# Kernel optimization log

Measured on AMD Instinct MI355X. Metric: run time of the kernel, lower is better.

## Reference

```python
import jax, jax.numpy as jnp
import numpy as np

N_ORDER = 13  # grid_size(10) + spline_order(3)
D_MODEL = 1024
HIDDEN = 2048
Z_DIM = 32
SEQ_LEN = 4096
IN0 = 2 * D_MODEL + Z_DIM  # 2080
RMS_EPS = 1e-6


def _kan_layer(x, base_w, poly_w, rms_scale):
    """KAN layer with Chebyshev basis, bf16 matmuls, fp32 RMSNorm.
    x: (..., in); base_w: (in,out); poly_w: (n_order,in,out); rms_scale: (out,)
    """
    prefix = x.shape[:-1]
    x2 = x.reshape(-1, x.shape[-1])
    out = jax.nn.silu(x2.astype(jnp.bfloat16)) @ base_w.astype(jnp.bfloat16)
    x_safe = jnp.tanh(x2.astype(jnp.float32))
    pw = poly_w.astype(jnp.bfloat16)
    T_prev = jnp.ones_like(x_safe)
    T_curr = x_safe
    out = out + T_prev.astype(jnp.bfloat16) @ pw[0]
    out = out + T_curr.astype(jnp.bfloat16) @ pw[1]
    for k in range(2, N_ORDER):
        T_next = 2.0 * x_safe * T_curr - T_prev
        out = out + T_next.astype(jnp.bfloat16) @ pw[k]
        T_prev, T_curr = T_curr, T_next
    o = out.astype(jnp.float32)
    o = o * jax.lax.rsqrt(jnp.mean(o * o, axis=-1, keepdims=True) + RMS_EPS) * rms_scale
    return o.reshape(prefix + (o.shape[-1],))


def setup_inputs() -> dict:
    key = jax.random.key(0)
    ks = jax.random.split(key, 10)
    B, N_tgt, S_ctx = 8, 2048, 128
    h_x = jax.random.normal(ks[0], (B, S_ctx, D_MODEL), dtype=jnp.float32)
    target_positions = jax.random.randint(ks[1], (B, N_tgt), 0, SEQ_LEN)
    z = jax.random.normal(ks[2], (B, N_tgt, Z_DIM), dtype=jnp.float32)
    pos_embed_w = jax.random.normal(ks[3], (SEQ_LEN, D_MODEL), dtype=jnp.float32) * 0.02
    base0 = jax.random.normal(ks[4], (IN0, HIDDEN), dtype=jnp.float32) * (1.0 / np.sqrt(IN0))
    poly0 = jax.random.normal(ks[5], (N_ORDER, IN0, HIDDEN), dtype=jnp.float32) * (0.1 / np.sqrt(IN0 * N_ORDER))
    rms0 = jnp.ones((HIDDEN,), dtype=jnp.float32)
    base1 = jax.random.normal(ks[6], (HIDDEN, D_MODEL), dtype=jnp.float32) * (1.0 / np.sqrt(HIDDEN))
    poly1 = jax.random.normal(ks[7], (N_ORDER, HIDDEN, D_MODEL), dtype=jnp.float32) * (0.1 / np.sqrt(HIDDEN * N_ORDER))
    rms1 = jnp.ones((D_MODEL,), dtype=jnp.float32)
    return {"h_x": h_x, "target_positions": target_positions, "z": z,
            "pos_embed_w": pos_embed_w, "base0": base0, "poly0": poly0, "rms0": rms0,
            "base1": base1, "poly1": poly1, "rms1": rms1}


def reference(h_x, target_positions, z, pos_embed_w, base0, poly0, rms0, base1, poly1, rms1):
    B = h_x.shape[0]
    N_tgt = target_positions.shape[1]
    ctx = jnp.broadcast_to(h_x[:, -1:, :], (B, N_tgt, D_MODEL))
    pos = pos_embed_w[target_positions]          # (B, N_tgt, d_model)
    x = jnp.concatenate([ctx, pos, z], axis=-1)  # (B, N_tgt, 2*d_model + z_dim)
    x = _kan_layer(x, base0, poly0, rms0)
    x = _kan_layer(x, base1, poly1, rms1)
    return x
```

## Files before the change

kernel.cpp:

```cpp
#include <hip/hip_runtime.h>
#include <hip/hip_bf16.h>
#include <math.h>

#define B_SZ 8
#define NT 2048
#define M_TOT (B_SZ * NT)
#define DM 1024
#define ZD 32
#define IN0 2080
#define HID 2048
#define OUT1 1024
#define NCH 13
#define PZ 1056
#define KPZ (NCH * PZ)
#define KCTX (NCH * DM)
#define K1 (NCH * HID)
#define RMS_EPS 1e-6f

typedef __bf16 bf16;
typedef __bf16 bf16x4 __attribute__((ext_vector_type(4)));
typedef __bf16 bf16x8 __attribute__((ext_vector_type(8)));
typedef float f32x4 __attribute__((ext_vector_type(4)));

__device__ __forceinline__ void gload16(const void* g, void* l) {
    __builtin_amdgcn_global_load_lds(
        (const __attribute__((address_space(1))) void*)g,
        (__attribute__((address_space(3))) void*)l, 16, 0, 0);
}

__device__ __forceinline__ float rb(float x) { return (float)(bf16)x; }

__device__ __forceinline__ unsigned pk2(float lo, float hi) {
    return (__builtin_bit_cast(unsigned, hi) & 0xFFFF0000u) |
           (__builtin_bit_cast(unsigned, lo) >> 16);
}
__device__ __forceinline__ float up_lo(unsigned u) { return __builtin_bit_cast(float, u << 16); }
__device__ __forceinline__ float up_hi(unsigned u) { return __builtin_bit_cast(float, u & 0xFFFF0000u); }

__global__ __launch_bounds__(256) void convert_w0(const float* __restrict__ base,
                                                  const float* __restrict__ poly,
                                                  bf16* __restrict__ wctx,
                                                  bf16* __restrict__ wposz) {
    __shared__ float tile[32][33];
    int c = blockIdx.z;
    const float* src = (c == 0) ? base : (poly + (size_t)c * IN0 * HID);
    int i0 = blockIdx.x * 32, n0 = blockIdx.y * 32;
    int tx = threadIdx.x, ty = threadIdx.y;
#pragma unroll
    for (int r = 0; r < 4; r++)
        tile[ty + r * 8][tx] = src[(size_t)(i0 + ty + r * 8) * HID + n0 + tx];
    __syncthreads();
#pragma unroll
    for (int r = 0; r < 4; r++) {
        int n = n0 + ty + r * 8;
        int i = i0 + tx;
        bf16 v = (bf16)tile[tx][ty + r * 8];
        if (i < 1024) wctx[(size_t)n * KCTX + (size_t)c * 1024 + i] = v;
        else          wposz[(size_t)n * KPZ + (size_t)c * PZ + (i - 1024)] = v;
    }
}

__global__ __launch_bounds__(256) void convert_w(const float* __restrict__ base,
                                                 const float* __restrict__ poly,
                                                 bf16* __restrict__ dst, int IN, int OUT) {
    __shared__ float tile[32][33];
    int c = blockIdx.z;
    const float* src = (c == 0) ? base : (poly + (size_t)c * IN * OUT);
    int i0 = blockIdx.x * 32, n0 = blockIdx.y * 32;
    int tx = threadIdx.x, ty = threadIdx.y;
#pragma unroll
    for (int r = 0; r < 4; r++)
        tile[ty + r * 8][tx] = src[(size_t)(i0 + ty + r * 8) * OUT + n0 + tx];
    __syncthreads();
    size_t ldd = (size_t)NCH * IN;
#pragma unroll
    for (int r = 0; r < 4; r++) {
        int n = n0 + ty + r * 8;
        int i = i0 + tx;
        dst[(size_t)n * ldd + (size_t)c * IN + i] = (bf16)tile[tx][ty + r * 8];
    }
}

__global__ void col_sum_s1(const float* __restrict__ w, float* __restrict__ partial,
                           int IN, int OUT) {
    __shared__ float sm[4][64];
    int tx = threadIdx.x, ty = threadIdx.y;
    int n = blockIdx.x * 64 + tx;
    int s = blockIdx.y;
    float acc = 0.f;
    for (int i = 4 * s + ty; i < IN; i += 128) acc += (float)(bf16)w[(size_t)i * OUT + n];
    sm[ty][tx] = acc;
    __syncthreads();
    if (ty == 0) partial[(size_t)s * OUT + n] = sm[0][tx] + sm[1][tx] + sm[2][tx] + sm[3][tx];
}
__global__ void col_sum_s2(const float* __restrict__ partial, float* __restrict__ bias, int OUT) {
    int n = blockIdx.x * 256 + threadIdx.x;
    if (n >= OUT) return;
    float s = 0.f;
#pragma unroll
    for (int k = 0; k < 32; k++) s += partial[(size_t)k * OUT + n];
    bias[n] = s;
}

__device__ __forceinline__ void write_features4(bf16* __restrict__ row, int i,
                                                float4 o, int stride) {
    float x[4] = {o.x, o.y, o.z, o.w};
    bf16x4 t;
#pragma unroll
    for (int l = 0; l < 4; l++) {
        float xb = rb(x[l]);
        float e  = rb(expf(-xb));
        float d  = rb(1.f + e);
        float sg = rb(1.f / d);
        t[l] = (bf16)(xb * sg);
    }
    *(bf16x4*)&row[i] = t;
    float xs[4], Tp[4], Tc[4];
#pragma unroll
    for (int l = 0; l < 4; l++) {
        xs[l] = tanhf(x[l]);
        Tp[l] = 1.f; Tc[l] = xs[l];
        t[l] = (bf16)xs[l];
    }
    *(bf16x4*)&row[(size_t)stride + i] = t;
#pragma unroll
    for (int k = 2; k < NCH; k++) {
#pragma unroll
        for (int l = 0; l < 4; l++) {
            float Tn = 2.f * xs[l] * Tc[l] - Tp[l];
            t[l] = (bf16)Tn;
            Tp[l] = Tc[l]; Tc[l] = Tn;
        }
        *(bf16x4*)&row[(size_t)k * stride + i] = t;
    }
}

__global__ __launch_bounds__(256) void build_fctx(const float* __restrict__ h_x,
                                                  bf16* __restrict__ Fctx) {
    int id = blockIdx.x * 256 + threadIdx.x;
    int b = id >> 8;
    int i = (id & 255) * 4;
    float4 v = *(const float4*)&h_x[((size_t)b * 128 + 127) * DM + i];
    write_features4(Fctx + (size_t)b * KCTX, i, v, DM);
}

__global__ void ctx_dot(const bf16* __restrict__ Fctx, const bf16* __restrict__ wctx,
                        float* __restrict__ ctx_part) {
    __shared__ float sm[4][64];
    int tx = threadIdx.x, ty = threadIdx.y;
    int n = blockIdx.x * 64 + tx;
    int c = blockIdx.y, b = blockIdx.z;
    const bf16* f = Fctx + ((size_t)b * NCH + c) * DM;
    const bf16* wv = wctx + (size_t)n * KCTX + (size_t)c * DM;
    float s = 0.f;
    for (int i = ty; i < DM; i += 4) s += (float)f[i] * (float)wv[i];
    sm[ty][tx] = s;
    __syncthreads();
    if (ty == 0) ctx_part[((size_t)b * NCH + c) * HID + n] = sm[0][tx] + sm[1][tx] + sm[2][tx] + sm[3][tx];
}

__global__ __launch_bounds__(256) void build_fposz(const int* __restrict__ tp,
                                                   const float* __restrict__ z,
                                                   const float* __restrict__ pe,
                                                   bf16* __restrict__ F) {
    int id = blockIdx.x * 256 + threadIdx.x;
    if (id >= M_TOT * (PZ / 4)) return;
    int ml = id / (PZ / 4);
    int i = (id - ml * (PZ / 4)) * 4;
    float4 v;
    if (i < DM) v = *(const float4*)&pe[(size_t)tp[ml] * DM + i];
    else v = *(const float4*)&z[(size_t)ml * ZD + (i - DM)];
    write_features4(F + (size_t)ml * KPZ, i, v, PZ);
}

__global__ __launch_bounds__(256) void rmsnorm_feat(const float* __restrict__ H,
                                                    const float* __restrict__ scale,
                                                    bf16* __restrict__ F) {
    constexpr int VPT = HID / (4 * 256);
    int row = blockIdx.x;
    const float4* p = (const float4*)(H + (size_t)row * HID);
    const float4* sc = (const float4*)scale;
    float4 v[VPT];
    float s = 0.f;
#pragma unroll
    for (int j = 0; j < VPT; j++) {
        v[j] = p[threadIdx.x + j * 256];
        s += v[j].x * v[j].x + v[j].y * v[j].y + v[j].z * v[j].z + v[j].w * v[j].w;
    }
#pragma unroll
    for (int o = 32; o > 0; o >>= 1) s += __shfl_down(s, o, 64);
    __shared__ float wsum[4];
    if ((threadIdx.x & 63) == 0) wsum[threadIdx.x >> 6] = s;
    __syncthreads();
    s = wsum[0] + wsum[1] + wsum[2] + wsum[3];
    float rs = rsqrtf(s * (1.0f / HID) + RMS_EPS);
    bf16* Frow = F + (size_t)row * K1;
#pragma unroll
    for (int j = 0; j < VPT; j++) {
        float4 sv = sc[threadIdx.x + j * 256];
        float4 o_;
        o_.x = v[j].x * rs * sv.x;
        o_.y = v[j].y * rs * sv.y;
        o_.z = v[j].z * rs * sv.z;
        o_.w = v[j].w * rs * sv.w;
        write_features4(Frow, (threadIdx.x + j * 256) * 4, o_, HID);
    }
}

template <int N>
__global__ __launch_bounds__(256) void rmsnorm_k(float* __restrict__ H,
                                                 const float* __restrict__ scale) {
    constexpr int VPT = N / (4 * 256);
    int row = blockIdx.x;
    float4* p = (float4*)(H + (size_t)row * N);
    const float4* sc = (const float4*)scale;
    float4 v[VPT];
    float s = 0.f;
#pragma unroll
    for (int j = 0; j < VPT; j++) {
        v[j] = p[threadIdx.x + j * 256];
        s += v[j].x * v[j].x + v[j].y * v[j].y + v[j].z * v[j].z + v[j].w * v[j].w;
    }
#pragma unroll
    for (int o = 32; o > 0; o >>= 1) s += __shfl_down(s, o, 64);
    __shared__ float wsum[4];
    if ((threadIdx.x & 63) == 0) wsum[threadIdx.x >> 6] = s;
    __syncthreads();
    s = wsum[0] + wsum[1] + wsum[2] + wsum[3];
    float rs = rsqrtf(s * (1.0f / N) + RMS_EPS);
#pragma unroll
    for (int j = 0; j < VPT; j++) {
        float4 sv = sc[threadIdx.x + j * 256];
        float4 o_;
        o_.x = v[j].x * rs * sv.x;
        o_.y = v[j].y * rs * sv.y;
        o_.z = v[j].z * rs * sv.z;
        o_.w = v[j].w * rs * sv.w;
        p[threadIdx.x + j * 256] = o_;
    }
}

#define BM 128
#define BN 128
#define BK 32
#define GROUP_M 8

__global__ __launch_bounds__(256, 4) void gemm_bias(const bf16* __restrict__ A,
                                                    const bf16* __restrict__ Bt,
                                                    const float* __restrict__ bias,
                                                    const float* __restrict__ ctxp,
                                                    float* __restrict__ C,
                                                    int Mrows, int N, int IN) {
    __shared__ __align__(16) bf16 As[BM * BK];
    __shared__ __align__(16) bf16 Bs[BN * BK];

    const int K = NCH * IN;
    int nbm = Mrows / BM, nbn = N / BN;
    int pid = blockIdx.x;
    int width = GROUP_M * nbn;
    int group_id = pid / width;
    int first_m = group_id * GROUP_M;
    int gsz = min(nbm - first_m, GROUP_M);
    int mb = first_m + (pid % width) % gsz;
    int nb = (pid % width) / gsz;

    int tid = threadIdx.x;
    int lane = tid & 63, wid = tid >> 6;
    int wm = wid >> 1, wn = wid & 1;

    const bf16* Ab = A + (size_t)mb * BM * K;
    const bf16* Bb = Bt + (size_t)nb * BN * K;

    const int q0 = tid, q1 = tid + 256;
    const int r0 = q0 >> 2, kk0 = (q0 & 3) * 8;
    const int r1 = q1 >> 2, kk1 = (q1 & 3) * 8;

    const int arow = wm * 64 + (lane & 15);
    const int brow = wn * 64 + (lane & 15);
    const int kqo = (lane >> 4) * 8;

    const int lcol = lane & 15, lrow4 = (lane >> 4) * 4;
    const int crow0 = mb * BM + wm * 64;
    const int ccol0 = nb * BN + wn * 64;
    const int b = (mb * BM) >> 11;

    unsigned outp[4][4][2] = {};

    for (int c = 0; c < NCH; c++) {
        f32x4 acc[4][4];
        if (ctxp) {
            const float* cp = ctxp + ((size_t)b * NCH + c) * N;
#pragma unroll
            for (int bn = 0; bn < 4; bn++) {
                float cv = cp[ccol0 + bn * 16 + lcol];
#pragma unroll
                for (int am = 0; am < 4; am++) acc[am][bn] = (f32x4){cv, cv, cv, cv};
            }
        } else {
#pragma unroll
            for (int am = 0; am < 4; am++)
#pragma unroll
                for (int bn = 0; bn < 4; bn++) acc[am][bn] = (f32x4){0.f, 0.f, 0.f, 0.f};
        }
        const size_t cb = (size_t)c * IN;
        for (int ks = 0; ks < IN; ks += BK) {
            const size_t kb = cb + ks;
            gload16(Ab + (size_t)r0 * K + kb + kk0, (char*)As + q0 * 16);
            gload16(Ab + (size_t)r1 * K + kb + kk1, (char*)As + q1 * 16);
            gload16(Bb + (size_t)r0 * K + kb + kk0, (char*)Bs + q0 * 16);
            gload16(Bb + (size_t)r1 * K + kb + kk1, (char*)Bs + q1 * 16);
            __syncthreads();

            bf16x8 af[4], bfr[4];
#pragma unroll
            for (int am = 0; am < 4; am++)
                af[am] = *(const bf16x8*)&As[(arow + am * 16) * BK + kqo];
#pragma unroll
            for (int bn = 0; bn < 4; bn++)
                bfr[bn] = *(const bf16x8*)&Bs[(brow + bn * 16) * BK + kqo];
#pragma unroll
            for (int am = 0; am < 4; am++)
#pragma unroll
                for (int bn = 0; bn < 4; bn++)
                    acc[am][bn] = __builtin_amdgcn_mfma_f32_16x16x32_bf16(af[am], bfr[bn], acc[am][bn], 0, 0, 0);
            __syncthreads();
        }
#pragma unroll
        for (int am = 0; am < 4; am++)
#pragma unroll
            for (int bn = 0; bn < 4; bn++)
#pragma unroll
                for (int ep = 0; ep < 2; ep++) {
                    float f0 = up_lo(outp[am][bn][ep]);
                    float f1 = up_hi(outp[am][bn][ep]);
                    f0 = rb(f0 + rb(acc[am][bn][ep * 2 + 0]));
                    f1 = rb(f1 + rb(acc[am][bn][ep * 2 + 1]));
                    outp[am][bn][ep] = pk2(f0, f1);
                }
        if (c == 0) {
#pragma unroll
            for (int bn = 0; bn < 4; bn++) {
                float bv = rb(bias[ccol0 + bn * 16 + lcol]);
#pragma unroll
                for (int am = 0; am < 4; am++)
#pragma unroll
                    for (int ep = 0; ep < 2; ep++) {
                        float f0 = rb(up_lo(outp[am][bn][ep]) + bv);
                        float f1 = rb(up_hi(outp[am][bn][ep]) + bv);
                        outp[am][bn][ep] = pk2(f0, f1);
                    }
            }
        }
    }

#pragma unroll
    for (int bn = 0; bn < 4; bn++) {
        int col = ccol0 + bn * 16 + lcol;
#pragma unroll
        for (int am = 0; am < 4; am++) {
            int row = crow0 + am * 16 + lrow4;
            C[(size_t)(row + 0) * N + col] = up_lo(outp[am][bn][0]);
            C[(size_t)(row + 1) * N + col] = up_hi(outp[am][bn][0]);
            C[(size_t)(row + 2) * N + col] = up_lo(outp[am][bn][1]);
            C[(size_t)(row + 3) * N + col] = up_hi(outp[am][bn][1]);
        }
    }
}

extern "C" void kernel_launch(void* const* d_in, const int* in_sizes, int n_in,
                              void* d_out, int out_size, void* d_ws, size_t ws_size,
                              hipStream_t stream) {
    const float* h_x   = (const float*)d_in[0];
    const int*   tp    = (const int*)d_in[1];
    const float* z     = (const float*)d_in[2];
    const float* pe    = (const float*)d_in[3];
    const float* base0 = (const float*)d_in[4];
    const float* poly0 = (const float*)d_in[5];
    const float* rms0  = (const float*)d_in[6];
    const float* base1 = (const float*)d_in[7];
    const float* poly1 = (const float*)d_in[8];
    const float* rms1  = (const float*)d_in[9];
    float* out = (float*)d_out;

    char* ws = (char*)d_ws;
    size_t off = 0;
    bf16* wctx  = (bf16*)(ws + off); off += (size_t)HID * KCTX * 2;
    bf16* wposz = (bf16*)(ws + off); off += (size_t)HID * KPZ * 2;
    bf16* wb1   = (bf16*)(ws + off); off += (size_t)OUT1 * K1 * 2;
    float* bias0 = (float*)(ws + off); off += HID * 4;
    float* bias1 = (float*)(ws + off); off += OUT1 * 4;
    float* partial = (float*)(ws + off); off += 32 * HID * 4;
    bf16* Fctx = (bf16*)(ws + off); off += (size_t)B_SZ * KCTX * 2;
    float* ctx_part = (float*)(ws + off); off += (size_t)B_SZ * NCH * HID * 4;
    float* H0 = (float*)(ws + off); off += (size_t)M_TOT * HID * 4;
    size_t fixed = off;

    bf16* FBIG = (bf16*)(ws + off);
    size_t avail = ws_size > fixed ? ws_size - fixed : 0;
    long long chunk_ll = (long long)(avail / ((size_t)K1 * 2));
    int chunk = (int)(chunk_ll > M_TOT ? M_TOT : chunk_ll);
    chunk &= ~127;
    if (chunk < 128) chunk = 128;

    dim3 tb(32, 8);
    convert_w0<<<dim3(IN0 / 32, HID / 32, NCH), tb, 0, stream>>>(base0, poly0, wctx, wposz);
    convert_w<<<dim3(HID / 32, OUT1 / 32, NCH), tb, 0, stream>>>(base1, poly1, wb1, HID, OUT1);
    col_sum_s1<<<dim3(HID / 64, 32), dim3(64, 4), 0, stream>>>(poly0, partial, IN0, HID);
    col_sum_s2<<<HID / 256, 256, 0, stream>>>(partial, bias0, HID);
    col_sum_s1<<<dim3(OUT1 / 64, 32), dim3(64, 4), 0, stream>>>(poly1, partial, HID, OUT1);
    col_sum_s2<<<OUT1 / 256, 256, 0, stream>>>(partial, bias1, OUT1);
    build_fctx<<<8, 256, 0, stream>>>(h_x, Fctx);
    ctx_dot<<<dim3(HID / 64, NCH, B_SZ), dim3(64, 4), 0, stream>>>(Fctx, wctx, ctx_part);
    bf16* Fposz = FBIG;
    build_fposz<<<(M_TOT * (PZ / 4) + 255) / 256, 256, 0, stream>>>(tp, z, pe, Fposz);
    gemm_bias<<<(M_TOT / BM) * (HID / BN), 256, 0, stream>>>(Fposz, wposz, bias0, ctx_part,
                                                             H0, M_TOT, HID, PZ);
    bf16* F1 = FBIG;
    for (int m0 = 0; m0 < M_TOT; m0 += chunk) {
        int rows = (M_TOT - m0 < chunk) ? (M_TOT - m0) : chunk;
        rmsnorm_feat<<<rows, 256, 0, stream>>>(H0 + (size_t)m0 * HID, rms0, F1);
        float* o = out + (size_t)m0 * OUT1;
        gemm_bias<<<(rows / BM) * (OUT1 / BN), 256, 0, stream>>>(F1, wb1, bias1, nullptr,
                                                                 o, rows, OUT1, HID);
        rmsnorm_k<OUT1><<<rows, 256, 0, stream>>>(o, rms1);
    }
}
```

Measured before the change: 3.933 ms.

## Precompute Chebyshev features per position table row and gather inside GEMM

Builds the Chebyshev feature expansion once per position-embedding row (4096 rows) and once per z row, then has the first GEMM gather A rows through target_positions directly, instead of materialising the full 16384-row feature matrix. This removes a large feature-build write and read. It also replaces the grouped-M tile ordering with an XCD-aware block remap. The price is scattered, non-contiguous A loads and a different L2 locality pattern for the weight tiles.

```diff
diff --git a/kernel.cpp b/kernel.cpp
--- a/kernel.cpp
+++ b/kernel.cpp
@@ -14,7 +14,10 @@
 #define PZ 1056
 #define KPZ (NCH * PZ)
 #define KCTX (NCH * DM)
+#define KPOS (NCH * DM)
+#define KZ (NCH * ZD)
 #define K1 (NCH * HID)
+#define NPOS 4096
 #define RMS_EPS 1e-6f
 
 typedef __bf16 bf16;
@@ -159,18 +162,23 @@
     if (ty == 0) ctx_part[((size_t)b * NCH + c) * HID + n] = sm[0][tx] + sm[1][tx] + sm[2][tx] + sm[3][tx];
 }
 
-__global__ __launch_bounds__(256) void build_fposz(const int* __restrict__ tp,
-                                                   const float* __restrict__ z,
-                                                   const float* __restrict__ pe,
-                                                   bf16* __restrict__ F) {
+__global__ __launch_bounds__(256) void build_fpos(const float* __restrict__ pe,
+                                                  bf16* __restrict__ Fpos) {
     int id = blockIdx.x * 256 + threadIdx.x;
-    if (id >= M_TOT * (PZ / 4)) return;
-    int ml = id / (PZ / 4);
-    int i = (id - ml * (PZ / 4)) * 4;
-    float4 v;
-    if (i < DM) v = *(const float4*)&pe[(size_t)tp[ml] * DM + i];
-    else v = *(const float4*)&z[(size_t)ml * ZD + (i - DM)];
-    write_features4(F + (size_t)ml * KPZ, i, v, PZ);
+    int p = id >> 8;
+    int i = (id & 255) * 4;
+    float4 v = *(const float4*)&pe[(size_t)p * DM + i];
+    write_features4(Fpos + (size_t)p * KPOS, i, v, DM);
+}
+
+__global__ __launch_bounds__(256) void build_fz(const float* __restrict__ z,
+                                                bf16* __restrict__ Fz) {
+    int id = blockIdx.x * 256 + threadIdx.x;
+    if (id >= M_TOT * (ZD / 4)) return;
+    int ml = id >> 3;
+    int i = (id & 7) * 4;
+    float4 v = *(const float4*)&z[(size_t)ml * ZD + i];
+    write_features4(Fz + (size_t)ml * KZ, i, v, ZD);
 }
 
 __global__ __launch_bounds__(256) void rmsnorm_feat(const float* __restrict__ H,
@@ -243,9 +251,11 @@
 #define BM 128
 #define BN 128
 #define BK 32
-#define GROUP_M 8
-
+
+template <int GATHER>
 __global__ __launch_bounds__(256, 4) void gemm_bias(const bf16* __restrict__ A,
+                                                    const bf16* __restrict__ Az,
+                                                    const int* __restrict__ tp,
                                                     const bf16* __restrict__ Bt,
                                                     const float* __restrict__ bias,
                                                     const float* __restrict__ ctxp,
@@ -255,25 +265,35 @@
     __shared__ __align__(16) bf16 Bs[BN * BK];
 
     const int K = NCH * IN;
-    int nbm = Mrows / BM, nbn = N / BN;
-    int pid = blockIdx.x;
-    int width = GROUP_M * nbn;
-    int group_id = pid / width;
-    int first_m = group_id * GROUP_M;
-    int gsz = min(nbm - first_m, GROUP_M);
-    int mb = first_m + (pid % width) % gsz;
-    int nb = (pid % width) / gsz;
+    const int nbm = Mrows / BM, nbn = N / BN;
+    {
+    }
+    int nwg = nbm * nbn;
+    int qq = nwg >> 3, rr = nwg & 7;
+    int xcd = blockIdx.x & 7, idx = blockIdx.x >> 3;
+    int wgid = (xcd < rr ? xcd * (qq + 1) : rr * (qq + 1) + (xcd - rr) * qq) + idx;
+    int mb = wgid / nbn, nb = wgid % nbn;
 
     int tid = threadIdx.x;
     int lane = tid & 63, wid = tid >> 6;
     int wm = wid >> 1, wn = wid & 1;
 
-    const bf16* Ab = A + (size_t)mb * BM * K;
-    const bf16* Bb = Bt + (size_t)nb * BN * K;
-
     const int q0 = tid, q1 = tid + 256;
     const int r0 = q0 >> 2, kk0 = (q0 & 3) * 8;
     const int r1 = q1 >> 2, kk1 = (q1 & 3) * 8;
+
+    const bf16 *a0, *a1, *z0 = nullptr, *z1 = nullptr;
+    if (GATHER) {
+        int row0 = mb * BM + r0, row1 = mb * BM + r1;
+        a0 = A + (size_t)tp[row0] * KPOS + kk0;
+        a1 = A + (size_t)tp[row1] * KPOS + kk1;
+        z0 = Az + (size_t)row0 * KZ + kk0;
+        z1 = Az + (size_t)row1 * KZ + kk1;
+    } else {
+        a0 = A + (size_t)(mb * BM + r0) * K + kk0;
+        a1 = A + (size_t)(mb * BM + r1) * K + kk1;
+    }
+    const bf16* Bb = Bt + (size_t)nb * BN * K;
 
     const int arow = wm * 64 + (lane & 15);
     const int brow = wn * 64 + (lane & 15);
@@ -288,7 +308,7 @@
 
     for (int c = 0; c < NCH; c++) {
         f32x4 acc[4][4];
-        if (ctxp) {
+        if (GATHER) {
             const float* cp = ctxp + ((size_t)b * NCH + c) * N;
 #pragma unroll
             for (int bn = 0; bn < 4; bn++) {
@@ -302,11 +322,18 @@
 #pragma unroll
                 for (int bn = 0; bn < 4; bn++) acc[am][bn] = (f32x4){0.f, 0.f, 0.f, 0.f};
         }
-        const size_t cb = (size_t)c * IN;
         for (int ks = 0; ks < IN; ks += BK) {
-            const size_t kb = cb + ks;
-            gload16(Ab + (size_t)r0 * K + kb + kk0, (char*)As + q0 * 16);
-            gload16(Ab + (size_t)r1 * K + kb + kk1, (char*)As + q1 * 16);
+            const bf16 *s0, *s1;
+            if (GATHER) {
+                if (ks < 1024) { s0 = a0 + c * 1024 + ks; s1 = a1 + c * 1024 + ks; }
+                else           { s0 = z0 + c * 32;        s1 = z1 + c * 32; }
+            } else {
+                s0 = a0 + (size_t)c * IN + ks;
+                s1 = a1 + (size_t)c * IN + ks;
+            }
+            gload16(s0, (char*)As + q0 * 16);
+            gload16(s1, (char*)As + q1 * 16);
+            const size_t kb = (size_t)c * IN + ks;
             gload16(Bb + (size_t)r0 * K + kb + kk0, (char*)Bs + q0 * 16);
             gload16(Bb + (size_t)r1 * K + kb + kk1, (char*)Bs + q1 * 16);
             __syncthreads();
@@ -392,10 +419,12 @@
     float* partial = (float*)(ws + off); off += 32 * HID * 4;
     bf16* Fctx = (bf16*)(ws + off); off += (size_t)B_SZ * KCTX * 2;
     float* ctx_part = (float*)(ws + off); off += (size_t)B_SZ * NCH * HID * 4;
+    bf16* Fpos = (bf16*)(ws + off); off += (size_t)NPOS * KPOS * 2;
+    bf16* Fz   = (bf16*)(ws + off); off += (size_t)M_TOT * KZ * 2;
     float* H0 = (float*)(ws + off); off += (size_t)M_TOT * HID * 4;
     size_t fixed = off;
 
-    bf16* FBIG = (bf16*)(ws + off);
+    bf16* F1 = (bf16*)(ws + off);
     size_t avail = ws_size > fixed ? ws_size - fixed : 0;
     long long chunk_ll = (long long)(avail / ((size_t)K1 * 2));
     int chunk = (int)(chunk_ll > M_TOT ? M_TOT : chunk_ll);
@@ -411,17 +440,16 @@
     col_sum_s2<<<OUT1 / 256, 256, 0, stream>>>(partial, bias1, OUT1);
     build_fctx<<<8, 256, 0, stream>>>(h_x, Fctx);
     ctx_dot<<<dim3(HID / 64, NCH, B_SZ), dim3(64, 4), 0, stream>>>(Fctx, wctx, ctx_part);
-    bf16* Fposz = FBIG;
-    build_fposz<<<(M_TOT * (PZ / 4) + 255) / 256, 256, 0, stream>>>(tp, z, pe, Fposz);
-    gemm_bias<<<(M_TOT / BM) * (HID / BN), 256, 0, stream>>>(Fposz, wposz, bias0, ctx_part,
-                                                             H0, M_TOT, HID, PZ);
-    bf16* F1 = FBIG;
+    build_fpos<<<NPOS, 256, 0, stream>>>(pe, Fpos);
+    build_fz<<<(M_TOT * (ZD / 4)) / 256, 256, 0, stream>>>(z, Fz);
+    gemm_bias<1><<<(M_TOT / BM) * (HID / BN), 256, 0, stream>>>(Fpos, Fz, tp, wposz, bias0,
+                                                                ctx_part, H0, M_TOT, HID, PZ);
     for (int m0 = 0; m0 < M_TOT; m0 += chunk) {
         int rows = (M_TOT - m0 < chunk) ? (M_TOT - m0) : chunk;
         rmsnorm_feat<<<rows, 256, 0, stream>>>(H0 + (size_t)m0 * HID, rms0, F1);
         float* o = out + (size_t)m0 * OUT1;
-        gemm_bias<<<(rows / BM) * (OUT1 / BN), 256, 0, stream>>>(F1, wb1, bias1, nullptr,
-                                                                 o, rows, OUT1, HID);
+        gemm_bias<0><<<(rows / BM) * (OUT1 / BN), 256, 0, stream>>>(F1, nullptr, nullptr, wb1,
+                                                                    bias1, nullptr, o, rows, OUT1, HID);
         rmsnorm_k<OUT1><<<rows, 256, 0, stream>>>(o, rms1);
     }
 }
```

Result: no change. 3.999 ms (+1.7%).
